# Performance work log

Measured on AMD Instinct MI355X. Metric: run time of the kernel, lower is better.

Reference implementation:

```python
import jax, jax.numpy as jnp
import numpy as np

N, D, E, P, L = 50000, 128, 800000, 9, 3
EPS = 1e-5  # torch nn.LayerNorm default eps


def _layernorm(x, g, b):
    m = jnp.mean(x, axis=-1, keepdims=True)
    v = jnp.mean((x - m) ** 2, axis=-1, keepdims=True)
    return (x - m) * jax.lax.rsqrt(v + EPS) * g + b


def _pol_transform(x, M, onehot):
    # x: (N,d), M: (P,d,d), onehot: (N,P). Equivalent to bmm(x[n] @ M[pol[n]])
    # without materializing the (N,d,d) gathered map tensor.
    return jnp.einsum('nd,np,pdk->nk', x, onehot, M)


def setup_inputs() -> dict:
    key = jax.random.key(0)
    ks = jax.random.split(key, 12)
    s = 1.0 / np.sqrt(D)  # xavier-ish scale
    f32 = jnp.float32
    return {
        'x': jax.random.normal(ks[0], (N, D), f32),
        'edge_index': jax.random.randint(ks[1], (2, E), 0, N),
        'ring_polarities': jax.random.randint(ks[2], (N,), 0, P),
        'Wr': jax.random.normal(ks[3], (L, D, D), f32) * s,          # restriction weights
        'S': jax.random.normal(ks[4], (L, P, D, D), f32) * s,        # send_maps
        'dS': jax.random.normal(ks[5], (L, P, D, D), f32) * 0.01,    # delta_send
        'R': jax.random.normal(ks[6], (L, P, D, D), f32) * s,        # receive_maps
        'dR': jax.random.normal(ks[7], (L, P, D, D), f32) * 0.01,    # delta_receive
        'res_scale': jnp.full((L,), 0.92, f32),
        'W1': jax.random.normal(ks[8], (L, D, D), f32) * s,          # update Linear 1
        'b1': jnp.zeros((L, D), f32),
        'ln_g': jnp.ones((L, D), f32),                               # update LayerNorm
        'ln_b': jnp.zeros((L, D), f32),
        'W2': jax.random.normal(ks[9], (L, D, D), f32) * s,          # update Linear 2
        'b2': jnp.zeros((L, D), f32),
        'norm_g': jnp.ones((L, D), f32),                             # output LayerNorm
        'norm_b': jnp.zeros((L, D), f32),
    }


def reference(x, edge_index, ring_polarities, Wr, S, dS, R, dR, res_scale,
              W1, b1, ln_g, ln_b, W2, b2, norm_g, norm_b):
    src, tgt = edge_index[0], edge_index[1]
    pol = ring_polarities % P
    onehot = jax.nn.one_hot(pol, P, dtype=x.dtype)  # (N,P)
    # deg is accumulated over row(=src) in the original code, then used to
    # normalize the scatter over col(=tgt) -- preserved faithfully.
    deg = jax.ops.segment_sum(jnp.ones((E,), x.dtype), src, num_segments=N)
    deg_norm = (1.0 / jnp.clip(deg, 1.0))[:, None]  # (N,1)

    residual = x
    for l in range(L):
        # send transform: map depends only on src-node polarity, so apply
        # per-node then gather (algebraically identical to per-edge bmm).
        xt = _pol_transform(x, S[l] + dS[l], onehot)          # (N,D)
        msg = xt[src] @ Wr[l].T                               # (E,D) restriction per edge
        agg = jax.ops.segment_sum(msg, tgt, num_segments=N)   # index_add scatter
        # receive transform depends only on tgt polarity; linear, so it
        # commutes with the sum over incoming edges.
        out = _pol_transform(agg, R[l] + dR[l], onehot) * deg_norm
        # update MLP (dropout inactive in eval)
        h = jax.nn.relu(_layernorm(out @ W1[l].T + b1[l], ln_g[l], ln_b[l]))
        out = h @ W2[l].T + b2[l]
        out = res_scale[l] * out + x                           # in==out residual
        x = _layernorm(out, norm_g[l], norm_b[l])
    return x + residual  # stack-level residual (res_proj is None, dims match)
```

## Files before the change

### kernel.cpp

```cpp
#include <hip/hip_runtime.h>
#include <hip/hip_bf16.h>

constexpr int N_ = 50000;
constexpr int D_ = 128;
constexpr int E_ = 800000;
constexpr int P_ = 9;
constexpr int L_ = 3;
constexpr float EPS_ = 1e-5f;

constexpr int TM = 64;
constexpr int CHUNK = 4096;
constexpr int NBK = (E_ + CHUNK - 1) / CHUNK;
constexpr int NBUK = 196;
constexpr int HHALF = 256 * NBK;
constexpr int HTOT = 2 * HHALF;
constexpr int NSB = HTOT / 1024;
constexpr int MAT = L_ * P_;

typedef short bf16x8 __attribute__((ext_vector_type(8)));
typedef float f32x4 __attribute__((ext_vector_type(4)));

#define GLD16(gp, lp)                                                        \
    __builtin_amdgcn_global_load_lds(                                        \
        (const __attribute__((address_space(1))) unsigned int*)(gp),         \
        (__attribute__((address_space(3))) unsigned int*)(lp), 16, 0, 0)

__device__ inline unsigned short f2bf(float f) {
    __hip_bfloat16 h = __float2bfloat16(f);
    return *reinterpret_cast<unsigned short*>(&h);
}
__device__ inline float bflo(unsigned u) { return __uint_as_float(u << 16); }
__device__ inline float bfhi(unsigned u) { return __uint_as_float(u & 0xffff0000u); }
__device__ inline float bf2f(unsigned short h) {
    return __uint_as_float((unsigned)h << 16);
}


__global__ __launch_bounds__(256) void setup_nk(const int* __restrict__ ring,
                                                int* __restrict__ pol,
                                                int* __restrict__ bcnt,
                                                const int* __restrict__ ei,
                                                int* __restrict__ histG) {
    __shared__ int h[P_];
    __shared__ int hT[256], hS[256];
    int blk = blockIdx.x, tid = threadIdx.x;
    if (tid < P_) h[tid] = 0;
    hT[tid] = 0;
    hS[tid] = 0;
    __syncthreads();
    int n = blk * 256 + tid;
    if (n < N_) {
        int p = ring[n] % P_;
        pol[n] = p;
        atomicAdd(&h[p], 1);
    }
    int base = blk * CHUNK;
#pragma unroll
    for (int i = 0; i < CHUNK / 256; ++i) {
        int e = base + tid + i * 256;
        if (e < E_) {
            atomicAdd(&hS[ei[e] >> 8], 1);
            atomicAdd(&hT[ei[E_ + e] >> 8], 1);
        }
    }
    __syncthreads();
    if (tid < P_ && h[tid] > 0) atomicAdd(&bcnt[tid], h[tid]);
    histG[tid * NBK + blk] = hT[tid];
    histG[HHALF + tid * NBK + blk] = hS[tid];
}


__global__ __launch_bounds__(1024) void scanH1(int* __restrict__ a,
                                               int* __restrict__ blkSum) {
    __shared__ int wsum[16];
    int tid = threadIdx.x, lane = tid & 63, wid = tid >> 6;
    int idx = blockIdx.x * 1024 + tid;
    int v = a[idx];
    int inc = v;
#pragma unroll
    for (int o = 1; o < 64; o <<= 1) {
        int t = __shfl_up(inc, o, 64);
        if (lane >= o) inc += t;
    }
    if (lane == 63) wsum[wid] = inc;
    __syncthreads();
    if (tid < 16) {
        int s = wsum[tid];
#pragma unroll
        for (int o = 1; o < 16; o <<= 1) {
            int t = __shfl_up(s, o, 64);
            if (tid >= o) s += t;
        }
        wsum[tid] = s;
    }
    __syncthreads();
    int wexcl = (wid == 0) ? 0 : wsum[wid - 1];
    a[idx] = wexcl + inc - v;
    if (tid == 1023) blkSum[blockIdx.x] = wsum[15];
}

__global__ void scanH2(const int* __restrict__ blkSum, int* __restrict__ blkOff,
                       int* __restrict__ offT, const int* __restrict__ bcnt,
                       int* __restrict__ boff, int* __restrict__ tileOff) {
    if (threadIdx.x != 0) return;
    int run = 0;
    for (int i = 0; i < NSB; ++i) {
        blkOff[i] = run;
        run += blkSum[i];
    }
    offT[N_] = E_;
    boff[0] = 0;
    tileOff[0] = 0;
    for (int p = 0; p < P_; ++p) {
        boff[p + 1] = boff[p] + bcnt[p];
        tileOff[p + 1] = tileOff[p] + (bcnt[p] + TM - 1) / TM;
    }
}

__global__ __launch_bounds__(1024) void scanH3(int* __restrict__ a,
                                               const int* __restrict__ blkOff) {
    int idx = blockIdx.x * 1024 + threadIdx.x;
    a[idx] += blkOff[blockIdx.x];
}


__global__ __launch_bounds__(256) void scatterTS(const int* __restrict__ ei,
                                                 const int* __restrict__ histG,
                                                 unsigned* __restrict__ bufT,
                                                 unsigned char* __restrict__ bufS8) {
    __shared__ int ldsT[256], ldsS[256];
    int blk = blockIdx.x, tid = threadIdx.x;
    ldsT[tid] = histG[tid * NBK + blk];
    ldsS[tid] = histG[HHALF + tid * NBK + blk] - E_;
    __syncthreads();
    int base = blk * CHUNK;
#pragma unroll
    for (int i = 0; i < CHUNK / 256; ++i) {
        int e = base + tid + i * 256;
        if (e < E_) {
            int s = ei[e], t = ei[E_ + e];
            int pT = atomicAdd(&ldsT[t >> 8], 1);
            bufT[pT] = ((unsigned)t << 16) | (unsigned)s;
            int pS = atomicAdd(&ldsS[s >> 8], 1);
            bufS8[pS] = (unsigned char)(s & 255);
        }
    }
}


__global__ __launch_bounds__(256) void finalize3(
    const unsigned* __restrict__ bufT, const unsigned char* __restrict__ bufS8,
    const int* __restrict__ histG, int* __restrict__ offT,
    unsigned short* __restrict__ eSrc, float* __restrict__ dnorm,
    const int* __restrict__ pol, const int* __restrict__ boff,
    int* __restrict__ bcur, int* __restrict__ blist) {
    __shared__ int s0[256];
    __shared__ int s1[256];
    int bb = blockIdx.x, tid = threadIdx.x;

    if (bb < NBUK) {
        int b = bb;
        int start = histG[b * NBK];
        int end = histG[(b + 1) * NBK];
        s0[tid] = 0;
        __syncthreads();
        for (int i = start + tid; i < end; i += 256)
            atomicAdd(&s0[(bufT[i] >> 16) & 255], 1);
        __syncthreads();
        if (tid < 64) {
            int b0 = 4 * tid;
            int v0 = s0[b0], v1 = s0[b0 + 1], v2 = s0[b0 + 2], v3 = s0[b0 + 3];
            int lsum = v0 + v1 + v2 + v3;
            int inc = lsum;
#pragma unroll
            for (int o = 1; o < 64; o <<= 1) {
                int t = __shfl_up(inc, o, 64);
                if (tid >= o) inc += t;
            }
            int excl = inc - lsum;
            s1[b0] = excl;
            s1[b0 + 1] = excl + v0;
            s1[b0 + 2] = excl + v0 + v1;
            s1[b0 + 3] = excl + v0 + v1 + v2;
        }
        __syncthreads();
        int node = (b << 8) + tid;
        if (node < N_) offT[node] = start + s1[tid];
        __syncthreads();
        for (int i = start + tid; i < end; i += 256) {
            unsigned pk = bufT[i];
            int pos = start + atomicAdd(&s1[(pk >> 16) & 255], 1);
            eSrc[pos] = (unsigned short)(pk & 0xFFFF);
        }
    } else if (bb < 2 * NBUK) {
        int b = bb - NBUK;
        int start = histG[HHALF + b * NBK] - E_;
        int end = histG[HHALF + (b + 1) * NBK] - E_;
        s0[tid] = 0;
        __syncthreads();
        for (int i = start + tid; i < end; i += 256) atomicAdd(&s0[bufS8[i]], 1);
        __syncthreads();
        int node = (b << 8) + tid;
        if (node < N_) {
            int dg = s0[tid];
            dnorm[node] = 1.f / (float)(dg > 1 ? dg : 1);
        }
    } else {
        int b = bb - 2 * NBUK;
        if (tid < P_) s0[tid] = 0;
        __syncthreads();
        int n = b * 256 + tid;
        int p = 0, loc = 0;
        bool act = (n < N_);
        if (act) {
            p = pol[n];
            loc = atomicAdd(&s0[p], 1);
        }
        __syncthreads();
        if (tid < P_ && s0[tid] > 0) s1[tid] = atomicAdd(&bcur[tid], s0[tid]);
        __syncthreads();
        if (act) blist[boff[p] + s1[p] + loc] = n;
    }
}


constexpr int GCONV = N_ * D_ / 4 / 256;
constexpr int GS = L_ * P_ * D_ * D_ / 256;
constexpr int GW2 = L_ * D_ * D_ / 256;
constexpr int GSPL = (MAT + 6) * 16384 / 256;
constexpr int GPREP = GCONV + 1 + GS + GW2 + GSPL;

__global__ __launch_bounds__(256) void prep_all(
    const float* __restrict__ x, unsigned short* __restrict__ xb,
    unsigned short* __restrict__ bufAb, unsigned short* __restrict__ bufBb,
    const float* __restrict__ S, const float* __restrict__ dS,
    unsigned short* __restrict__ Sb,
    const float* __restrict__ W2, unsigned short* __restrict__ W2b,
    const float* __restrict__ R, const float* __restrict__ dR,
    const float* __restrict__ W1, const float* __restrict__ Wr,
    unsigned short* __restrict__ Arh, unsigned short* __restrict__ Arl,
    unsigned short* __restrict__ W1h, unsigned short* __restrict__ W1l,
    unsigned short* __restrict__ Wrth, unsigned short* __restrict__ Wrtl) {
    int b = blockIdx.x, tid = threadIdx.x;
    if (b < GCONV) {
        int i = b * 256 + tid;
        float4 v = ((const float4*)x)[i];
        ushort4 o;
        o.x = f2bf(v.x); o.y = f2bf(v.y); o.z = f2bf(v.z); o.w = f2bf(v.w);
        ((ushort4*)xb)[i] = o;
    } else if (b < GCONV + 1) {
        if (tid < 64) {
            ((unsigned*)(xb + (size_t)N_ * D_))[tid] = 0;
            ((unsigned*)(bufAb + (size_t)N_ * D_))[tid] = 0;
            ((unsigned*)(bufBb + (size_t)N_ * D_))[tid] = 0;
        }
    } else if (b < GCONV + 1 + GS) {
        int idx = (b - GCONV - 1) * 256 + tid;
        int base = idx / (D_ * D_);
        int rem = idx % (D_ * D_);
        int c = rem / D_, d = rem % D_;
        size_t in = (size_t)base * D_ * D_ + (size_t)d * D_ + c;
        Sb[idx] = f2bf(S[in] + dS[in]);
    } else if (b < GCONV + 1 + GS + GW2) {
        int idx = (b - GCONV - 1 - GS) * 256 + tid;
        W2b[idx] = f2bf(W2[idx]);
    } else {
        constexpr int SZ1 = MAT * 16384;
        constexpr int SZ2 = SZ1 + 3 * 16384;
        int idx = (b - GCONV - 1 - GS - GW2) * 256 + tid;
        float v;
        unsigned short* oh;
        unsigned short* ol;
        int j;
        if (idx < SZ1) {
            v = R[idx] + dR[idx];
            oh = Arh; ol = Arl; j = idx;
        } else if (idx < SZ2) {
            j = idx - SZ1;
            v = W1[j];
            oh = W1h; ol = W1l;
        } else {
            j = idx - SZ2;
            int l = j >> 14, rem = j & 16383;
            int d = rem >> 7, i = rem & 127;
            v = Wr[(l << 14) + i * 128 + d];
            oh = Wrth; ol = Wrtl;
        }
        unsigned short h = f2bf(v);
        oh[j] = h;
        ol[j] = f2bf(v - bf2f(h));
    }
}


template <bool APM, bool BPM, bool OUT_SPLIT>
__global__ __launch_bounds__(256) void small_mfma(
    const unsigned short* __restrict__ Ah, const unsigned short* __restrict__ Al,
    const unsigned short* __restrict__ Bh, const unsigned short* __restrict__ Bl,
    unsigned short* __restrict__ Oh, unsigned short* __restrict__ Ol) {
    __shared__ unsigned short stg[(OUT_SPLIT ? 2 : 1) * 64 * 136];
    int tid = threadIdx.x, b = blockIdx.x;
    int mat = b >> 1, rb = b & 1;
    int l = mat / P_;
    size_t aoff = (size_t)(APM ? mat : l) * 16384 + (size_t)rb * 8192;
    size_t boff = (size_t)(BPM ? mat : l) * 16384;
    const unsigned short* ahp = Ah + aoff;
    const unsigned short* alp = Al + aoff;
    const unsigned short* bhp = Bh + boff;
    const unsigned short* blp = Bl + boff;

    int lane = tid & 63, wave = tid >> 6;
    int n = lane & 15, q = lane >> 4;
    int wr = wave * 16;

    f32x4 acc[8];
#pragma unroll
    for (int t = 0; t < 8; ++t) acc[t] = (f32x4){0.f, 0.f, 0.f, 0.f};

    int arow = (wr + n) * 128;
#pragma unroll
    for (int kc = 0; kc < 4; ++kc) {
        int ko = kc * 32 + q * 8;
        bf16x8 avh = *(const bf16x8*)(ahp + arow + ko);
        bf16x8 avl = *(const bf16x8*)(alp + arow + ko);
#pragma unroll
        for (int t = 0; t < 8; ++t) {
            int brow = (t * 16 + n) * 128;
            bf16x8 bvh = *(const bf16x8*)(bhp + brow + ko);
            bf16x8 bvl = *(const bf16x8*)(blp + brow + ko);
            acc[t] = __builtin_amdgcn_mfma_f32_16x16x32_bf16(avh, bvh, acc[t], 0, 0, 0);
            acc[t] = __builtin_amdgcn_mfma_f32_16x16x32_bf16(avh, bvl, acc[t], 0, 0, 0);
            acc[t] = __builtin_amdgcn_mfma_f32_16x16x32_bf16(avl, bvh, acc[t], 0, 0, 0);
        }
    }
#pragma unroll
    for (int t = 0; t < 8; ++t)
#pragma unroll
        for (int r = 0; r < 4; ++r) {
            int row = wr + q * 4 + r;
            float v = acc[t][r];
            unsigned short h = f2bf(v);
            stg[row * 136 + t * 16 + n] = h;
            if constexpr (OUT_SPLIT)
                stg[64 * 136 + row * 136 + t * 16 + n] = f2bf(v - bf2f(h));
        }
    __syncthreads();
    size_t obase = (size_t)mat * 16384 + (size_t)rb * 8192;
#pragma unroll
    for (int i = 0; i < 4; ++i) {
        int c = tid + i * 256;
        int r = c >> 4, off = c & 15;
        *(uint4*)(Oh + obase + r * 128 + off * 8) =
            *(const uint4*)(stg + r * 136 + off * 8);
        if constexpr (OUT_SPLIT)
            *(uint4*)(Ol + obase + r * 128 + off * 8) =
                *(const uint4*)(stg + 64 * 136 + r * 136 + off * 8);
    }
}


__device__ inline void accum_row(float* acc, uint4 r) {
    acc[0] += bflo(r.x); acc[1] += bfhi(r.x);
    acc[2] += bflo(r.y); acc[3] += bfhi(r.y);
    acc[4] += bflo(r.z); acc[5] += bfhi(r.z);
    acc[6] += bflo(r.w); acc[7] += bfhi(r.w);
}

__global__ __launch_bounds__(256) void aggregate_bf(const unsigned short* __restrict__ xt,
                                                    const int* __restrict__ offT,
                                                    const unsigned short* __restrict__ eSrc,
                                                    unsigned short* __restrict__ agg) {
    int nd = blockIdx.x * 4 + (threadIdx.x >> 6);
    if (nd >= N_) return;
    int l = threadIdx.x & 63;
    int g = l >> 4, c16 = l & 15;
    int beg = offT[nd], end = offT[nd + 1];

    float acc[8];
#pragma unroll
    for (int k = 0; k < 8; ++k) acc[k] = 0.f;

    for (int base = beg; base < end; base += 64) {
        int cnt = min(64, end - base);
        int idxv = (l < cnt) ? (int)eSrc[base + l] : 0;
        int steps = (cnt + 3) >> 2;
        int j = 0;
        for (; j + 3 < steps; j += 4) {
            int e0 = 4 * j + g, e1 = e0 + 4, e2 = e0 + 8, e3 = e0 + 12;
            int i0 = __shfl(idxv, e0, 64);
            int i1 = __shfl(idxv, e1, 64);
            int i2 = __shfl(idxv, e2, 64);
            int i3 = __shfl(idxv, e3, 64);
            int r0 = (e0 < cnt) ? i0 : N_;
            int r1 = (e1 < cnt) ? i1 : N_;
            int r2 = (e2 < cnt) ? i2 : N_;
            int r3 = (e3 < cnt) ? i3 : N_;
            uint4 v0 = ((const uint4*)(xt + (size_t)r0 * D_))[c16];
            uint4 v1 = ((const uint4*)(xt + (size_t)r1 * D_))[c16];
            uint4 v2 = ((const uint4*)(xt + (size_t)r2 * D_))[c16];
            uint4 v3 = ((const uint4*)(xt + (size_t)r3 * D_))[c16];
            accum_row(acc, v0);
            accum_row(acc, v1);
            accum_row(acc, v2);
            accum_row(acc, v3);
        }
        for (; j < steps; ++j) {
            int e0 = 4 * j + g;
            int i0 = __shfl(idxv, e0, 64);
            int r0 = (e0 < cnt) ? i0 : N_;
            uint4 v0 = ((const uint4*)(xt + (size_t)r0 * D_))[c16];
            accum_row(acc, v0);
        }
    }
#pragma unroll
    for (int k = 0; k < 8; ++k) {
        acc[k] += __shfl_xor(acc[k], 16, 64);
        acc[k] += __shfl_xor(acc[k], 32, 64);
    }
    if (g == 0) {
        uint4 o;
        o.x = (unsigned)f2bf(acc[0]) | ((unsigned)f2bf(acc[1]) << 16);
        o.y = (unsigned)f2bf(acc[2]) | ((unsigned)f2bf(acc[3]) << 16);
        o.z = (unsigned)f2bf(acc[4]) | ((unsigned)f2bf(acc[5]) << 16);
        o.w = (unsigned)f2bf(acc[6]) | ((unsigned)f2bf(acc[7]) << 16);
        ((uint4*)(agg + (size_t)nd * D_))[c16] = o;
    }
}


__device__ inline void stage_B_async(const unsigned short* __restrict__ B,
                                     unsigned short* sB, int wave, int lane) {
    int rsub = lane >> 4, cl = lane & 15;
#pragma unroll
    for (int j = 0; j < 8; ++j) {
        int seg = wave * 8 + j;
        int row = seg * 4 + rsub;
        GLD16(B + row * 128 + ((cl ^ (row & 15)) << 3), sB + seg * 512);
    }
}

__device__ inline void stage_A_async(const unsigned short* __restrict__ A,
                                     const int* rid, unsigned short* sA,
                                     int wave, int lane) {
    int rsub = lane >> 4, cl = lane & 15;
#pragma unroll
    for (int j = 0; j < 4; ++j) {
        int seg = wave * 4 + j;
        int rloc = seg * 4 + rsub;
        int rw = rid[rloc];
        size_t grow = (rw >= 0) ? (size_t)rw : (size_t)N_;
        GLD16(A + grow * 128 + ((cl ^ (rloc & 15)) << 3), sA + seg * 512);
    }
}


__global__ __launch_bounds__(256) void gemm_xt0(
    const unsigned short* __restrict__ A, const unsigned short* __restrict__ Bw,
    unsigned short* __restrict__ OutB, const int* __restrict__ blist,
    const int* __restrict__ boff, const int* __restrict__ tileOff) {
    __shared__ unsigned short sB[128 * 128];
    __shared__ unsigned short sA[64 * 128];
    __shared__ int rid[TM];
    int tid = threadIdx.x, b = blockIdx.x;
    if (b >= tileOff[P_]) return;
    int pp = 0;
    while (pp < P_ - 1 && b >= tileOff[pp + 1]) ++pp;
    int tb = b - tileOff[pp];
    int cnt = boff[pp + 1] - boff[pp];
    int nrows = min(TM, cnt - tb * TM);
    int rowbase = boff[pp] + tb * TM;

    if (tid < TM)
        rid[tid] = (tid < nrows) ? blist[rowbase + tid] : -1;
    __syncthreads();

    int lane = tid & 63, wave = tid >> 6;
    stage_B_async(Bw + (size_t)pp * D_ * D_, sB, wave, lane);
    stage_A_async(A, rid, sA, wave, lane);
    __syncthreads();

    int n = lane & 15, q = lane >> 4, wr = wave * 16;

    f32x4 acc[8];
#pragma unroll
    for (int t = 0; t < 8; ++t) acc[t] = (f32x4){0.f, 0.f, 0.f, 0.f};
#pragma unroll
    for (int kc = 0; kc < 4; ++kc) {
        int cs = (((kc << 2) + q) ^ n) << 3;
        bf16x8 af = *(const bf16x8*)(sA + (wr + n) * 128 + cs);
#pragma unroll
        for (int t = 0; t < 8; ++t) {
            bf16x8 bf = *(const bf16x8*)(sB + (t * 16 + n) * 128 + cs);
            acc[t] = __builtin_amdgcn_mfma_f32_16x16x32_bf16(af, bf, acc[t], 0, 0, 0);
        }
    }
    __syncthreads();
#pragma unroll
    for (int t = 0; t < 8; ++t)
#pragma unroll
        for (int r = 0; r < 4; ++r) {
            int rl = q * 4 + r;
            int c = ((t * 16 + n) >> 3);
            sA[(wr + rl) * 128 + ((c ^ rl) << 3) + (n & 7)] = f2bf(acc[t][r]);
        }
    __syncthreads();
#pragma unroll
    for (int i = 0; i < 4; ++i) {
        int cth = tid + i * 256;
        int r = cth >> 4, cl = cth & 15;
        int row = rid[r];
        if (row >= 0)
            *(uint4*)(OutB + (size_t)row * D_ + (cl << 3)) =
                *(const uint4*)(sA + r * 128 + ((cl ^ (r & 15)) << 3));
    }
}


template <bool LAST>
__global__ __launch_bounds__(256) void fused_layer(
    const unsigned short* __restrict__ agg, const unsigned short* __restrict__ DmAll,
    const unsigned short* __restrict__ W2b, const unsigned short* __restrict__ SnAll,
    const int* __restrict__ blist, const int* __restrict__ boff,
    const int* __restrict__ tileOff, const float* __restrict__ dnorm,
    const float* __restrict__ b1v, const float* __restrict__ g1v,
    const float* __restrict__ e1v, const float* __restrict__ b2v,
    const float* __restrict__ g2v, const float* __restrict__ e2v,
    const float* __restrict__ rs_ptr, const float* __restrict__ xres,
    const float* __restrict__ x0add, float* __restrict__ OutF,
    unsigned short* __restrict__ OutXt) {
    __shared__ unsigned short sB[128 * 128];
    __shared__ unsigned short sA[64 * 128];
    __shared__ int rid[TM];
    __shared__ float dnRow[TM];

    int tid = threadIdx.x, b = blockIdx.x;
    if (b >= tileOff[P_]) return;
    int pp = 0;
    while (pp < P_ - 1 && b >= tileOff[pp + 1]) ++pp;
    int tb = b - tileOff[pp];
    int cnt = boff[pp + 1] - boff[pp];
    int nrows = min(TM, cnt - tb * TM);
    int rowbase = boff[pp] + tb * TM;

    if (tid < TM) {
        int r = (tid < nrows) ? blist[rowbase + tid] : -1;
        rid[tid] = r;
        dnRow[tid] = (r >= 0) ? dnorm[r] : 1.f;
    }
    __syncthreads();

    int lane = tid & 63, wave = tid >> 6;
    stage_B_async(DmAll + (size_t)pp * D_ * D_, sB, wave, lane);
    stage_A_async(agg, rid, sA, wave, lane);

    int n = lane & 15, q = lane >> 4, wr = wave * 16;

    int rowid[4];
    float dn4[4];
#pragma unroll
    for (int r = 0; r < 4; ++r) {
        int rr = wr + q * 4 + r;
        rowid[r] = rid[rr];
        dn4[r] = dnRow[rr];
    }

    float xr[8][4];
#pragma unroll
    for (int t = 0; t < 8; ++t) {
        int col = t * 16 + n;
#pragma unroll
        for (int r = 0; r < 4; ++r)
            xr[t][r] = (rowid[r] >= 0) ? xres[(size_t)rowid[r] * D_ + col] : 0.f;
    }
    __syncthreads();

    f32x4 acc[8];
#pragma unroll
    for (int t = 0; t < 8; ++t) acc[t] = (f32x4){0.f, 0.f, 0.f, 0.f};
#pragma unroll
    for (int kc = 0; kc < 4; ++kc) {
        int cs = (((kc << 2) + q) ^ n) << 3;
        bf16x8 af = *(const bf16x8*)(sA + (wr + n) * 128 + cs);
#pragma unroll
        for (int t = 0; t < 8; ++t) {
            bf16x8 bf = *(const bf16x8*)(sB + (t * 16 + n) * 128 + cs);
            acc[t] = __builtin_amdgcn_mfma_f32_16x16x32_bf16(af, bf, acc[t], 0, 0, 0);
        }
    }

    {
        float rs1[4] = {0, 0, 0, 0}, rs2[4] = {0, 0, 0, 0};
#pragma unroll
        for (int t = 0; t < 8; ++t) {
            int col = t * 16 + n;
            float bia = b1v[col];
#pragma unroll
            for (int r = 0; r < 4; ++r) {
                float v = dn4[r] * acc[t][r] + bia;
                acc[t][r] = v;
                rs1[r] += v;
                rs2[r] += v * v;
            }
        }
#pragma unroll
        for (int mk = 1; mk < 16; mk <<= 1)
#pragma unroll
            for (int r = 0; r < 4; ++r) {
                rs1[r] += __shfl_xor(rs1[r], mk, 64);
                rs2[r] += __shfl_xor(rs2[r], mk, 64);
            }
        float mr[4], rv[4];
#pragma unroll
        for (int r = 0; r < 4; ++r) {
            float mm = rs1[r] * (1.f / 128.f);
            mr[r] = mm;
            rv[r] = rsqrtf(rs2[r] * (1.f / 128.f) - mm * mm + EPS_);
        }
#pragma unroll
        for (int t = 0; t < 8; ++t) {
            int col = t * 16 + n;
            float gg = g1v[col], bbv = e1v[col];
#pragma unroll
            for (int r = 0; r < 4; ++r)
                acc[t][r] = fmaxf((acc[t][r] - mr[r]) * rv[r] * gg + bbv, 0.f);
        }
    }

    __syncthreads();
    stage_B_async(W2b, sB, wave, lane);
#pragma unroll
    for (int t = 0; t < 8; ++t)
#pragma unroll
        for (int r = 0; r < 4; ++r) {
            int rl = q * 4 + r;
            int c = ((t * 16 + n) >> 3);
            sA[(wr + rl) * 128 + ((c ^ rl) << 3) + (n & 7)] = f2bf(acc[t][r]);
        }
    __syncthreads();

#pragma unroll
    for (int t = 0; t < 8; ++t) acc[t] = (f32x4){0.f, 0.f, 0.f, 0.f};
#pragma unroll
    for (int kc = 0; kc < 4; ++kc) {
        int cs = (((kc << 2) + q) ^ n) << 3;
        bf16x8 af = *(const bf16x8*)(sA + (wr + n) * 128 + cs);
#pragma unroll
        for (int t = 0; t < 8; ++t) {
            bf16x8 bf = *(const bf16x8*)(sB + (t * 16 + n) * 128 + cs);
            acc[t] = __builtin_amdgcn_mfma_f32_16x16x32_bf16(af, bf, acc[t], 0, 0, 0);
        }
    }

    {
        float rs = rs_ptr[0];
        float rs1[4] = {0, 0, 0, 0}, rs2[4] = {0, 0, 0, 0};
#pragma unroll
        for (int t = 0; t < 8; ++t) {
            int col = t * 16 + n;
            float bia = b2v[col];
#pragma unroll
            for (int r = 0; r < 4; ++r) {
                float v = rs * (acc[t][r] + bia) + xr[t][r];
                acc[t][r] = v;
                rs1[r] += v;
                rs2[r] += v * v;
            }
        }
#pragma unroll
        for (int mk = 1; mk < 16; mk <<= 1)
#pragma unroll
            for (int r = 0; r < 4; ++r) {
                rs1[r] += __shfl_xor(rs1[r], mk, 64);
                rs2[r] += __shfl_xor(rs2[r], mk, 64);
            }
        float mr[4], rv[4];
#pragma unroll
        for (int r = 0; r < 4; ++r) {
            float mm = rs1[r] * (1.f / 128.f);
            mr[r] = mm;
            rv[r] = rsqrtf(rs2[r] * (1.f / 128.f) - mm * mm + EPS_);
        }
#pragma unroll
        for (int t = 0; t < 8; ++t) {
            int col = t * 16 + n;
            float gg = g2v[col], bbv = e2v[col];
#pragma unroll
            for (int r = 0; r < 4; ++r) {
                float nv = (acc[t][r] - mr[r]) * rv[r] * gg + bbv;
                if constexpr (LAST) {
                    if (rowid[r] >= 0) nv += x0add[(size_t)rowid[r] * D_ + col];
                }
                acc[t][r] = nv;
                if (rowid[r] >= 0) OutF[(size_t)rowid[r] * D_ + col] = nv;
            }
        }
    }

    if constexpr (!LAST) {
        __syncthreads();
        stage_B_async(SnAll + (size_t)pp * D_ * D_, sB, wave, lane);
#pragma unroll
        for (int t = 0; t < 8; ++t)
#pragma unroll
            for (int r = 0; r < 4; ++r) {
                int rl = q * 4 + r;
                int c = ((t * 16 + n) >> 3);
                sA[(wr + rl) * 128 + ((c ^ rl) << 3) + (n & 7)] = f2bf(acc[t][r]);
            }
        __syncthreads();

#pragma unroll
        for (int t = 0; t < 8; ++t) acc[t] = (f32x4){0.f, 0.f, 0.f, 0.f};
#pragma unroll
        for (int kc = 0; kc < 4; ++kc) {
            int cs = (((kc << 2) + q) ^ n) << 3;
            bf16x8 af = *(const bf16x8*)(sA + (wr + n) * 128 + cs);
#pragma unroll
            for (int t = 0; t < 8; ++t) {
                bf16x8 bf = *(const bf16x8*)(sB + (t * 16 + n) * 128 + cs);
                acc[t] = __builtin_amdgcn_mfma_f32_16x16x32_bf16(af, bf, acc[t], 0, 0, 0);
            }
        }
#pragma unroll
        for (int t = 0; t < 8; ++t)
#pragma unroll
            for (int r = 0; r < 4; ++r) {
                int rl = q * 4 + r;
                int c = ((t * 16 + n) >> 3);
                sA[(wr + rl) * 128 + ((c ^ rl) << 3) + (n & 7)] = f2bf(acc[t][r]);
            }
        __syncthreads();
#pragma unroll
        for (int i = 0; i < 4; ++i) {
            int cth = tid + i * 256;
            int r = cth >> 4, cl = cth & 15;
            int row = rid[r];
            if (row >= 0)
                *(uint4*)(OutXt + (size_t)row * D_ + (cl << 3)) =
                    *(const uint4*)(sA + r * 128 + ((cl ^ (r & 15)) << 3));
        }
    }
}


extern "C" void kernel_launch(void* const* d_in, const int* in_sizes, int n_in,
                              void* d_out, int out_size, void* d_ws, size_t ws_size,
                              hipStream_t stream) {
    const float* x0 = (const float*)d_in[0];
    const int* ei = (const int*)d_in[1];
    const int* ring = (const int*)d_in[2];
    const float* Wr = (const float*)d_in[3];
    const float* S = (const float*)d_in[4];
    const float* dS = (const float*)d_in[5];
    const float* R = (const float*)d_in[6];
    const float* dR = (const float*)d_in[7];
    const float* rsc = (const float*)d_in[8];
    const float* W1 = (const float*)d_in[9];
    const float* b1 = (const float*)d_in[10];
    const float* lng = (const float*)d_in[11];
    const float* lnb = (const float*)d_in[12];
    const float* W2 = (const float*)d_in[13];
    const float* b2 = (const float*)d_in[14];
    const float* ng = (const float*)d_in[15];
    const float* nb = (const float*)d_in[16];
    float* out = (float*)d_out;

    char* w = (char*)d_ws;
    auto alloc = [&](size_t bytes) {
        char* p = w;
        w += (bytes + 15) & ~(size_t)15;
        return p;
    };
    unsigned short* xb = (unsigned short*)alloc((size_t)(N_ + 1) * D_ * 2);
    unsigned short* bufAb = (unsigned short*)alloc((size_t)(N_ + 1) * D_ * 2);
    unsigned short* bufBb = (unsigned short*)alloc((size_t)(N_ + 1) * D_ * 2);
    float* xbuf = (float*)alloc((size_t)N_ * D_ * 4);
    unsigned short* Sb = (unsigned short*)alloc((size_t)L_ * P_ * D_ * D_ * 2);
    unsigned short* Dmb = (unsigned short*)alloc((size_t)L_ * P_ * D_ * D_ * 2);
    unsigned short* W2b = (unsigned short*)alloc((size_t)L_ * D_ * D_ * 2);
    unsigned short* Arh = (unsigned short*)alloc((size_t)MAT * 16384 * 2);
    unsigned short* Arl = (unsigned short*)alloc((size_t)MAT * 16384 * 2);
    unsigned short* W1h = (unsigned short*)alloc((size_t)3 * 16384 * 2);
    unsigned short* W1l = (unsigned short*)alloc((size_t)3 * 16384 * 2);
    unsigned short* Wrth = (unsigned short*)alloc((size_t)3 * 16384 * 2);
    unsigned short* Wrtl = (unsigned short*)alloc((size_t)3 * 16384 * 2);
    unsigned short* T1th = (unsigned short*)alloc((size_t)MAT * 16384 * 2);
    unsigned short* T1tl = (unsigned short*)alloc((size_t)MAT * 16384 * 2);
    float* dnorm = (float*)alloc((size_t)N_ * 4);
    int* histG = (int*)alloc((size_t)HTOT * 4);
    unsigned* bufT = (unsigned*)alloc((size_t)E_ * 4);
    unsigned char* bufS8 = (unsigned char*)alloc((size_t)E_);
    unsigned short* eSrc = (unsigned short*)alloc((size_t)E_ * 2);
    int* offT = (int*)alloc((size_t)(N_ + 1) * 4);
    int* pol = (int*)alloc((size_t)N_ * 4);
    int* boff = (int*)alloc((size_t)(P_ + 1) * 4);
    int* tileOff = (int*)alloc((size_t)(P_ + 1) * 4);
    int* blist = (int*)alloc((size_t)N_ * 4);
    int* blkSum = (int*)alloc((size_t)NSB * 4);
    int* blkOff = (int*)alloc((size_t)NSB * 4);
    int* bcnt = (int*)alloc((size_t)2 * P_ * 4);
    int* bcur = bcnt + P_;

    hipMemsetAsync(bcnt, 0, (size_t)2 * P_ * 4, stream);

    const int BTILES = N_ / TM + P_;

    setup_nk<<<NBK, 256, 0, stream>>>(ring, pol, bcnt, ei, histG);
    scanH1<<<NSB, 1024, 0, stream>>>(histG, blkSum);
    scanH2<<<1, 64, 0, stream>>>(blkSum, blkOff, offT, bcnt, boff, tileOff);
    scanH3<<<NSB, 1024, 0, stream>>>(histG, blkOff);
    scatterTS<<<NBK, 256, 0, stream>>>(ei, histG, bufT, bufS8);
    finalize3<<<3 * NBUK, 256, 0, stream>>>(bufT, bufS8, histG, offT, eSrc, dnorm,
                                            pol, boff, bcur, blist);
    prep_all<<<GPREP, 256, 0, stream>>>(x0, xb, bufAb, bufBb, S, dS, Sb, W2, W2b,
                                        R, dR, W1, Wr, Arh, Arl, W1h, W1l, Wrth, Wrtl);
    small_mfma<false, true, true><<<2 * MAT, 256, 0, stream>>>(
        W1h, W1l, Arh, Arl, T1th, T1tl);
    small_mfma<true, false, false><<<2 * MAT, 256, 0, stream>>>(
        T1th, T1tl, Wrth, Wrtl, Dmb, nullptr);

    gemm_xt0<<<BTILES, 256, 0, stream>>>(xb, Sb, bufAb, blist, boff, tileOff);

    for (int l = 0; l < L_; ++l) {
        const size_t lPDD = (size_t)l * P_ * D_ * D_;
        const size_t lDD = (size_t)l * D_ * D_;
        const size_t lD = (size_t)l * D_;
        aggregate_bf<<<N_ / 4, 256, 0, stream>>>(bufAb, offT, eSrc, bufBb);
        const float* xr = (l == 0) ? x0 : xbuf;
        if (l < L_ - 1) {
            fused_layer<false><<<BTILES, 256, 0, stream>>>(
                bufBb, Dmb + lPDD, W2b + lDD, Sb + lPDD + (size_t)P_ * D_ * D_,
                blist, boff, tileOff, dnorm,
                b1 + lD, lng + lD, lnb + lD, b2 + lD, ng + lD, nb + lD,
                rsc + l, xr, nullptr, xbuf, bufAb);
        } else {
            fused_layer<true><<<BTILES, 256, 0, stream>>>(
                bufBb, Dmb + lPDD, W2b + lDD, nullptr,
                blist, boff, tileOff, dnorm,
                b1 + lD, lng + lD, lnb + lD, b2 + lD, ng + lD, nb + lD,
                rsc + l, xr, x0, out, nullptr);
        }
    }
}
```

Baseline: 378.6 us.

## Store node features in polarity-sorted order and read GEMM weights from global

Nodes are renumbered into polarity-bucket order through a new perm array. The features, residual buffer, degree norms and edge source indices are all permuted once during prep, and aggregation writes its result at the permuted position. As a result the GEMM tiles load contiguous rows instead of gathering through blist. The per-tile weight matrices are now read straight from global memory rather than staged in LDS, and most block-wide barriers are replaced by per-wave waits, since each wave only touches its own rows. This removes the indirect gathers and cuts LDS use. The cost is repeated uncached-in-LDS weight reads per wave and an extra permutation pass over the edges.

New measurement: 464.0 us. 22.5% more time.

```diff
diff --git a/kernel.cpp b/kernel.cpp
--- a/kernel.cpp
+++ b/kernel.cpp
@@ -153,7 +153,7 @@
     const int* __restrict__ histG, int* __restrict__ offT,
     unsigned short* __restrict__ eSrc, float* __restrict__ dnorm,
     const int* __restrict__ pol, const int* __restrict__ boff,
-    int* __restrict__ bcur, int* __restrict__ blist) {
+    int* __restrict__ bcur, int* __restrict__ blist, int* __restrict__ perm) {
     __shared__ int s0[256];
     __shared__ int s1[256];
     int bb = blockIdx.x, tid = threadIdx.x;
@@ -219,20 +219,29 @@
         __syncthreads();
         if (tid < P_ && s0[tid] > 0) s1[tid] = atomicAdd(&bcur[tid], s0[tid]);
         __syncthreads();
-        if (act) blist[boff[p] + s1[p] + loc] = n;
+        if (act) {
+            int pos = boff[p] + s1[p] + loc;
+            blist[pos] = n;
+            perm[n] = pos;
+        }
     }
 }
 
 
 constexpr int GCONV = N_ * D_ / 4 / 256;
+constexpr int GDN = (N_ + 255) / 256;
+constexpr int GER = (E_ + 255) / 256;
 constexpr int GS = L_ * P_ * D_ * D_ / 256;
 constexpr int GW2 = L_ * D_ * D_ / 256;
 constexpr int GSPL = (MAT + 6) * 16384 / 256;
-constexpr int GPREP = GCONV + 1 + GS + GW2 + GSPL;
+constexpr int GPREP = GCONV + 1 + GDN + GER + GS + GW2 + GSPL;
 
 __global__ __launch_bounds__(256) void prep_all(
-    const float* __restrict__ x, unsigned short* __restrict__ xb,
-    unsigned short* __restrict__ bufAb, unsigned short* __restrict__ bufBb,
+    const float* __restrict__ x, const int* __restrict__ perm,
+    const int* __restrict__ blist, unsigned short* __restrict__ xbP,
+    float* __restrict__ xbufP, unsigned short* __restrict__ bufAb,
+    const float* __restrict__ dnorm, float* __restrict__ dnormp,
+    unsigned short* __restrict__ eSrc,
     const float* __restrict__ S, const float* __restrict__ dS,
     unsigned short* __restrict__ Sb,
     const float* __restrict__ W2, unsigned short* __restrict__ W2b,
@@ -244,30 +253,35 @@
     int b = blockIdx.x, tid = threadIdx.x;
     if (b < GCONV) {
         int i = b * 256 + tid;
+        int n = i >> 5, g4 = i & 31;
+        int pr = perm[n];
         float4 v = ((const float4*)x)[i];
         ushort4 o;
         o.x = f2bf(v.x); o.y = f2bf(v.y); o.z = f2bf(v.z); o.w = f2bf(v.w);
-        ((ushort4*)xb)[i] = o;
+        ((ushort4*)(xbP + (size_t)pr * D_))[g4] = o;
+        ((float4*)(xbufP + (size_t)pr * D_))[g4] = v;
     } else if (b < GCONV + 1) {
-        if (tid < 64) {
-            ((unsigned*)(xb + (size_t)N_ * D_))[tid] = 0;
-            ((unsigned*)(bufAb + (size_t)N_ * D_))[tid] = 0;
-            ((unsigned*)(bufBb + (size_t)N_ * D_))[tid] = 0;
-        }
-    } else if (b < GCONV + 1 + GS) {
-        int idx = (b - GCONV - 1) * 256 + tid;
+        if (tid < 64) ((unsigned*)(bufAb + (size_t)N_ * D_))[tid] = 0;
+    } else if (b < GCONV + 1 + GDN) {
+        int i = (b - GCONV - 1) * 256 + tid;
+        if (i < N_) dnormp[i] = dnorm[blist[i]];
+    } else if (b < GCONV + 1 + GDN + GER) {
+        int e = (b - GCONV - 1 - GDN) * 256 + tid;
+        if (e < E_) eSrc[e] = (unsigned short)perm[eSrc[e]];
+    } else if (b < GCONV + 1 + GDN + GER + GS) {
+        int idx = (b - GCONV - 1 - GDN - GER) * 256 + tid;
         int base = idx / (D_ * D_);
         int rem = idx % (D_ * D_);
         int c = rem / D_, d = rem % D_;
         size_t in = (size_t)base * D_ * D_ + (size_t)d * D_ + c;
         Sb[idx] = f2bf(S[in] + dS[in]);
-    } else if (b < GCONV + 1 + GS + GW2) {
-        int idx = (b - GCONV - 1 - GS) * 256 + tid;
+    } else if (b < GCONV + 1 + GDN + GER + GS + GW2) {
+        int idx = (b - GCONV - 1 - GDN - GER - GS) * 256 + tid;
         W2b[idx] = f2bf(W2[idx]);
     } else {
         constexpr int SZ1 = MAT * 16384;
         constexpr int SZ2 = SZ1 + 3 * 16384;
-        int idx = (b - GCONV - 1 - GS - GW2) * 256 + tid;
+        int idx = (b - GCONV - 1 - GDN - GER - GS - GW2) * 256 + tid;
         float v;
         unsigned short* oh;
         unsigned short* ol;
@@ -369,7 +383,8 @@
 __global__ __launch_bounds__(256) void aggregate_bf(const unsigned short* __restrict__ xt,
                                                     const int* __restrict__ offT,
                                                     const unsigned short* __restrict__ eSrc,
-                                                    unsigned short* __restrict__ agg) {
+                                                    unsigned short* __restrict__ agg,
+                                                    const int* __restrict__ perm) {
     int nd = blockIdx.x * 4 + (threadIdx.x >> 6);
     if (nd >= N_) return;
     int l = threadIdx.x & 63;
@@ -418,49 +433,35 @@
         acc[k] += __shfl_xor(acc[k], 32, 64);
     }
     if (g == 0) {
+        int pnd = perm[nd];
         uint4 o;
         o.x = (unsigned)f2bf(acc[0]) | ((unsigned)f2bf(acc[1]) << 16);
         o.y = (unsigned)f2bf(acc[2]) | ((unsigned)f2bf(acc[3]) << 16);
         o.z = (unsigned)f2bf(acc[4]) | ((unsigned)f2bf(acc[5]) << 16);
         o.w = (unsigned)f2bf(acc[6]) | ((unsigned)f2bf(acc[7]) << 16);
-        ((uint4*)(agg + (size_t)nd * D_))[c16] = o;
-    }
-}
-
-
-__device__ inline void stage_B_async(const unsigned short* __restrict__ B,
-                                     unsigned short* sB, int wave, int lane) {
-    int rsub = lane >> 4, cl = lane & 15;
-#pragma unroll
-    for (int j = 0; j < 8; ++j) {
-        int seg = wave * 8 + j;
-        int row = seg * 4 + rsub;
-        GLD16(B + row * 128 + ((cl ^ (row & 15)) << 3), sB + seg * 512);
-    }
-}
-
-__device__ inline void stage_A_async(const unsigned short* __restrict__ A,
-                                     const int* rid, unsigned short* sA,
-                                     int wave, int lane) {
+        ((uint4*)(agg + (size_t)pnd * D_))[c16] = o;
+    }
+}
+
+
+__device__ inline void stage_A_contig(const unsigned short* __restrict__ A,
+                                      int rowbase, unsigned short* sA,
+                                      int wave, int lane) {
     int rsub = lane >> 4, cl = lane & 15;
 #pragma unroll
     for (int j = 0; j < 4; ++j) {
         int seg = wave * 4 + j;
         int rloc = seg * 4 + rsub;
-        int rw = rid[rloc];
-        size_t grow = (rw >= 0) ? (size_t)rw : (size_t)N_;
-        GLD16(A + grow * 128 + ((cl ^ (rloc & 15)) << 3), sA + seg * 512);
-    }
-}
-
+        GLD16(A + (size_t)(rowbase + rloc) * D_ + ((cl ^ (rloc & 15)) << 3),
+              sA + seg * 512);
+    }
+}
 
 __global__ __launch_bounds__(256) void gemm_xt0(
     const unsigned short* __restrict__ A, const unsigned short* __restrict__ Bw,
-    unsigned short* __restrict__ OutB, const int* __restrict__ blist,
-    const int* __restrict__ boff, const int* __restrict__ tileOff) {
-    __shared__ unsigned short sB[128 * 128];
+    unsigned short* __restrict__ OutB, const int* __restrict__ boff,
+    const int* __restrict__ tileOff) {
     __shared__ unsigned short sA[64 * 128];
-    __shared__ int rid[TM];
     int tid = threadIdx.x, b = blockIdx.x;
     if (b >= tileOff[P_]) return;
     int pp = 0;
@@ -470,16 +471,12 @@
     int nrows = min(TM, cnt - tb * TM);
     int rowbase = boff[pp] + tb * TM;
 
-    if (tid < TM)
-        rid[tid] = (tid < nrows) ? blist[rowbase + tid] : -1;
-    __syncthreads();
-
     int lane = tid & 63, wave = tid >> 6;
-    stage_B_async(Bw + (size_t)pp * D_ * D_, sB, wave, lane);
-    stage_A_async(A, rid, sA, wave, lane);
-    __syncthreads();
+    stage_A_contig(A, rowbase, sA, wave, lane);
+    const unsigned short* Bp = Bw + (size_t)pp * D_ * D_;
 
     int n = lane & 15, q = lane >> 4, wr = wave * 16;
+    __builtin_amdgcn_s_waitcnt(0);
 
     f32x4 acc[8];
 #pragma unroll
@@ -488,51 +485,45 @@
     for (int kc = 0; kc < 4; ++kc) {
         int cs = (((kc << 2) + q) ^ n) << 3;
         bf16x8 af = *(const bf16x8*)(sA + (wr + n) * 128 + cs);
+        int ko = kc * 32 + q * 8;
 #pragma unroll
         for (int t = 0; t < 8; ++t) {
-            bf16x8 bf = *(const bf16x8*)(sB + (t * 16 + n) * 128 + cs);
-            acc[t] = __builtin_amdgcn_mfma_f32_16x16x32_bf16(af, bf, acc[t], 0, 0, 0);
-        }
-    }
-    __syncthreads();
+            bf16x8 bv = *(const bf16x8*)(Bp + (t * 16 + n) * 128 + ko);
+            acc[t] = __builtin_amdgcn_mfma_f32_16x16x32_bf16(af, bv, acc[t], 0, 0, 0);
+        }
+    }
 #pragma unroll
     for (int t = 0; t < 8; ++t)
 #pragma unroll
         for (int r = 0; r < 4; ++r) {
             int rl = q * 4 + r;
-            int c = ((t * 16 + n) >> 3);
+            int c = (t * 16 + n) >> 3;
             sA[(wr + rl) * 128 + ((c ^ rl) << 3) + (n & 7)] = f2bf(acc[t][r]);
         }
-    __syncthreads();
-#pragma unroll
-    for (int i = 0; i < 4; ++i) {
-        int cth = tid + i * 256;
-        int r = cth >> 4, cl = cth & 15;
-        int row = rid[r];
-        if (row >= 0)
-            *(uint4*)(OutB + (size_t)row * D_ + (cl << 3)) =
-                *(const uint4*)(sA + r * 128 + ((cl ^ (r & 15)) << 3));
-    }
-}
-
+    int rl2 = lane >> 2, cb = lane & 3;
+    if (rl2 < nrows - wr) {
+#pragma unroll
+        for (int i = 0; i < 4; ++i) {
+            int c = i * 4 + cb;
+            uint4 v = *(const uint4*)(sA + (wr + rl2) * 128 + ((c ^ rl2) << 3));
+            *(uint4*)(OutB + (size_t)(rowbase + wr + rl2) * D_ + (c << 3)) = v;
+        }
+    }
+}
 
 template <bool LAST>
 __global__ __launch_bounds__(256) void fused_layer(
     const unsigned short* __restrict__ agg, const unsigned short* __restrict__ DmAll,
     const unsigned short* __restrict__ W2b, const unsigned short* __restrict__ SnAll,
-    const int* __restrict__ blist, const int* __restrict__ boff,
-    const int* __restrict__ tileOff, const float* __restrict__ dnorm,
+    const int* __restrict__ boff, const int* __restrict__ tileOff,
+    const int* __restrict__ blist, const float* __restrict__ dnormp,
     const float* __restrict__ b1v, const float* __restrict__ g1v,
     const float* __restrict__ e1v, const float* __restrict__ b2v,
     const float* __restrict__ g2v, const float* __restrict__ e2v,
-    const float* __restrict__ rs_ptr, const float* __restrict__ xres,
-    const float* __restrict__ x0add, float* __restrict__ OutF,
+    const float* __restrict__ rs_ptr, const float* __restrict__ xresP,
+    const float* __restrict__ x0, float* __restrict__ OutF,
     unsigned short* __restrict__ OutXt) {
-    __shared__ unsigned short sB[128 * 128];
     __shared__ unsigned short sA[64 * 128];
-    __shared__ int rid[TM];
-    __shared__ float dnRow[TM];
-
     int tid = threadIdx.x, b = blockIdx.x;
     if (b >= tileOff[P_]) return;
     int pp = 0;
@@ -542,37 +533,16 @@
     int nrows = min(TM, cnt - tb * TM);
     int rowbase = boff[pp] + tb * TM;
 
-    if (tid < TM) {
-        int r = (tid < nrows) ? blist[rowbase + tid] : -1;
-        rid[tid] = r;
-        dnRow[tid] = (r >= 0) ? dnorm[r] : 1.f;
-    }
-    __syncthreads();
-
     int lane = tid & 63, wave = tid >> 6;
-    stage_B_async(DmAll + (size_t)pp * D_ * D_, sB, wave, lane);
-    stage_A_async(agg, rid, sA, wave, lane);
+    stage_A_contig(agg, rowbase, sA, wave, lane);
 
     int n = lane & 15, q = lane >> 4, wr = wave * 16;
-
-    int rowid[4];
+    const unsigned short* Bp = DmAll + (size_t)pp * D_ * D_;
     float dn4[4];
 #pragma unroll
-    for (int r = 0; r < 4; ++r) {
-        int rr = wr + q * 4 + r;
-        rowid[r] = rid[rr];
-        dn4[r] = dnRow[rr];
-    }
-
-    float xr[8][4];
-#pragma unroll
-    for (int t = 0; t < 8; ++t) {
-        int col = t * 16 + n;
-#pragma unroll
-        for (int r = 0; r < 4; ++r)
-            xr[t][r] = (rowid[r] >= 0) ? xres[(size_t)rowid[r] * D_ + col] : 0.f;
-    }
-    __syncthreads();
+    for (int r = 0; r < 4; ++r) dn4[r] = dnormp[rowbase + wr + q * 4 + r];
+
+    __builtin_amdgcn_s_waitcnt(0);
 
     f32x4 acc[8];
 #pragma unroll
@@ -581,10 +551,11 @@
     for (int kc = 0; kc < 4; ++kc) {
         int cs = (((kc << 2) + q) ^ n) << 3;
         bf16x8 af = *(const bf16x8*)(sA + (wr + n) * 128 + cs);
+        int ko = kc * 32 + q * 8;
 #pragma unroll
         for (int t = 0; t < 8; ++t) {
-            bf16x8 bf = *(const bf16x8*)(sB + (t * 16 + n) * 128 + cs);
-            acc[t] = __builtin_amdgcn_mfma_f32_16x16x32_bf16(af, bf, acc[t], 0, 0, 0);
+            bf16x8 bv = *(const bf16x8*)(Bp + (t * 16 + n) * 128 + ko);
+            acc[t] = __builtin_amdgcn_mfma_f32_16x16x32_bf16(af, bv, acc[t], 0, 0, 0);
         }
     }
 
@@ -626,17 +597,14 @@
         }
     }
 
-    __syncthreads();
-    stage_B_async(W2b, sB, wave, lane);
 #pragma unroll
     for (int t = 0; t < 8; ++t)
 #pragma unroll
         for (int r = 0; r < 4; ++r) {
             int rl = q * 4 + r;
-            int c = ((t * 16 + n) >> 3);
+            int c = (t * 16 + n) >> 3;
             sA[(wr + rl) * 128 + ((c ^ rl) << 3) + (n & 7)] = f2bf(acc[t][r]);
         }
-    __syncthreads();
 
 #pragma unroll
     for (int t = 0; t < 8; ++t) acc[t] = (f32x4){0.f, 0.f, 0.f, 0.f};
@@ -644,10 +612,11 @@
     for (int kc = 0; kc < 4; ++kc) {
         int cs = (((kc << 2) + q) ^ n) << 3;
         bf16x8 af = *(const bf16x8*)(sA + (wr + n) * 128 + cs);
+        int ko = kc * 32 + q * 8;
 #pragma unroll
         for (int t = 0; t < 8; ++t) {
-            bf16x8 bf = *(const bf16x8*)(sB + (t * 16 + n) * 128 + cs);
-            acc[t] = __builtin_amdgcn_mfma_f32_16x16x32_bf16(af, bf, acc[t], 0, 0, 0);
+            bf16x8 bv = *(const bf16x8*)(W2b + (t * 16 + n) * 128 + ko);
+            acc[t] = __builtin_amdgcn_mfma_f32_16x16x32_bf16(af, bv, acc[t], 0, 0, 0);
         }
     }
 
@@ -660,7 +629,9 @@
             float bia = b2v[col];
 #pragma unroll
             for (int r = 0; r < 4; ++r) {
-                float v = rs * (acc[t][r] + bia) + xr[t][r];
+                int row = wr + q * 4 + r;
+                float v = rs * (acc[t][r] + bia) +
+                          xresP[(size_t)(rowbase + row) * D_ + col];
                 acc[t][r] = v;
                 rs1[r] += v;
                 rs2[r] += v * v;
@@ -680,45 +651,64 @@
             mr[r] = mm;
             rv[r] = rsqrtf(rs2[r] * (1.f / 128.f) - mm * mm + EPS_);
         }
-#pragma unroll
-        for (int t = 0; t < 8; ++t) {
-            int col = t * 16 + n;
-            float gg = g2v[col], bbv = e2v[col];
+        if constexpr (LAST) {
+            int rowid[4];
 #pragma unroll
             for (int r = 0; r < 4; ++r) {
-                float nv = (acc[t][r] - mr[r]) * rv[r] * gg + bbv;
-                if constexpr (LAST) {
-                    if (rowid[r] >= 0) nv += x0add[(size_t)rowid[r] * D_ + col];
+                int rl = wr + q * 4 + r;
+                rowid[r] = (rl < nrows) ? blist[rowbase + rl] : -1;
+            }
+#pragma unroll
+            for (int t = 0; t < 8; ++t) {
+                int col = t * 16 + n;
+                float gg = g2v[col], bbv = e2v[col];
+#pragma unroll
+                for (int r = 0; r < 4; ++r) {
+                    if (rowid[r] >= 0) {
+                        float nv = (acc[t][r] - mr[r]) * rv[r] * gg + bbv +
+                                   x0[(size_t)rowid[r] * D_ + col];
+                        OutF[(size_t)rowid[r] * D_ + col] = nv;
+                    }
                 }
-                acc[t][r] = nv;
-                if (rowid[r] >= 0) OutF[(size_t)rowid[r] * D_ + col] = nv;
+            }
+        } else {
+#pragma unroll
+            for (int t = 0; t < 8; ++t) {
+                int col = t * 16 + n;
+                float gg = g2v[col], bbv = e2v[col];
+#pragma unroll
+                for (int r = 0; r < 4; ++r) {
+                    int row = wr + q * 4 + r;
+                    float nv = (acc[t][r] - mr[r]) * rv[r] * gg + bbv;
+                    acc[t][r] = nv;
+                    if (row < nrows)
+                        OutF[(size_t)(rowbase + row) * D_ + col] = nv;
+                }
             }
         }
     }
 
     if constexpr (!LAST) {
-        __syncthreads();
-        stage_B_async(SnAll + (size_t)pp * D_ * D_, sB, wave, lane);
+        const unsigned short* Sn = SnAll + (size_t)pp * D_ * D_;
 #pragma unroll
         for (int t = 0; t < 8; ++t)
 #pragma unroll
             for (int r = 0; r < 4; ++r) {
                 int rl = q * 4 + r;
-                int c = ((t * 16 + n) >> 3);
+                int c = (t * 16 + n) >> 3;
                 sA[(wr + rl) * 128 + ((c ^ rl) << 3) + (n & 7)] = f2bf(acc[t][r]);
             }
-        __syncthreads();
-
 #pragma unroll
         for (int t = 0; t < 8; ++t) acc[t] = (f32x4){0.f, 0.f, 0.f, 0.f};
 #pragma unroll
         for (int kc = 0; kc < 4; ++kc) {
             int cs = (((kc << 2) + q) ^ n) << 3;
             bf16x8 af = *(const bf16x8*)(sA + (wr + n) * 128 + cs);
+            int ko = kc * 32 + q * 8;
 #pragma unroll
             for (int t = 0; t < 8; ++t) {
-                bf16x8 bf = *(const bf16x8*)(sB + (t * 16 + n) * 128 + cs);
-                acc[t] = __builtin_amdgcn_mfma_f32_16x16x32_bf16(af, bf, acc[t], 0, 0, 0);
+                bf16x8 bv = *(const bf16x8*)(Sn + (t * 16 + n) * 128 + ko);
+                acc[t] = __builtin_amdgcn_mfma_f32_16x16x32_bf16(af, bv, acc[t], 0, 0, 0);
             }
         }
 #pragma unroll
@@ -726,18 +716,17 @@
 #pragma unroll
             for (int r = 0; r < 4; ++r) {
                 int rl = q * 4 + r;
-                int c = ((t * 16 + n) >> 3);
+                int c = (t * 16 + n) >> 3;
                 sA[(wr + rl) * 128 + ((c ^ rl) << 3) + (n & 7)] = f2bf(acc[t][r]);
             }
-        __syncthreads();
-#pragma unroll
-        for (int i = 0; i < 4; ++i) {
-            int cth = tid + i * 256;
-            int r = cth >> 4, cl = cth & 15;
-            int row = rid[r];
-            if (row >= 0)
-                *(uint4*)(OutXt + (size_t)row * D_ + (cl << 3)) =
-                    *(const uint4*)(sA + r * 128 + ((cl ^ (r & 15)) << 3));
+        int rl2 = lane >> 2, cb = lane & 3;
+        if (rl2 < nrows - wr) {
+#pragma unroll
+            for (int i = 0; i < 4; ++i) {
+                int c = i * 4 + cb;
+                uint4 v = *(const uint4*)(sA + (wr + rl2) * 128 + ((c ^ rl2) << 3));
+                *(uint4*)(OutXt + (size_t)(rowbase + wr + rl2) * D_ + (c << 3)) = v;
+            }
         }
     }
 }
@@ -771,10 +760,11 @@
         w += (bytes + 15) & ~(size_t)15;
         return p;
     };
-    unsigned short* xb = (unsigned short*)alloc((size_t)(N_ + 1) * D_ * 2);
-    unsigned short* bufAb = (unsigned short*)alloc((size_t)(N_ + 1) * D_ * 2);
-    unsigned short* bufBb = (unsigned short*)alloc((size_t)(N_ + 1) * D_ * 2);
-    float* xbuf = (float*)alloc((size_t)N_ * D_ * 4);
+    const size_t NP = (size_t)(N_ + 64);
+    unsigned short* xbP = (unsigned short*)alloc(NP * D_ * 2);
+    unsigned short* bufAb = (unsigned short*)alloc(NP * D_ * 2);
+    unsigned short* bufBb = (unsigned short*)alloc(NP * D_ * 2);
+    float* xbufP = (float*)alloc(NP * D_ * 4);
     unsigned short* Sb = (unsigned short*)alloc((size_t)L_ * P_ * D_ * D_ * 2);
     unsigned short* Dmb = (unsigned short*)alloc((size_t)L_ * P_ * D_ * D_ * 2);
     unsigned short* W2b = (unsigned short*)alloc((size_t)L_ * D_ * D_ * 2);
@@ -787,6 +777,7 @@
     unsigned short* T1th = (unsigned short*)alloc((size_t)MAT * 16384 * 2);
     unsigned short* T1tl = (unsigned short*)alloc((size_t)MAT * 16384 * 2);
     float* dnorm = (float*)alloc((size_t)N_ * 4);
+    float* dnormp = (float*)alloc(NP * 4);
     int* histG = (int*)alloc((size_t)HTOT * 4);
     unsigned* bufT = (unsigned*)alloc((size_t)E_ * 4);
     unsigned char* bufS8 = (unsigned char*)alloc((size_t)E_);
@@ -796,6 +787,7 @@
     int* boff = (int*)alloc((size_t)(P_ + 1) * 4);
     int* tileOff = (int*)alloc((size_t)(P_ + 1) * 4);
     int* blist = (int*)alloc((size_t)N_ * 4);
+    int* perm = (int*)alloc((size_t)N_ * 4);
     int* blkSum = (int*)alloc((size_t)NSB * 4);
     int* blkOff = (int*)alloc((size_t)NSB * 4);
     int* bcnt = (int*)alloc((size_t)2 * P_ * 4);
@@ -811,34 +803,34 @@
     scanH3<<<NSB, 1024, 0, stream>>>(histG, blkOff);
     scatterTS<<<NBK, 256, 0, stream>>>(ei, histG, bufT, bufS8);
     finalize3<<<3 * NBUK, 256, 0, stream>>>(bufT, bufS8, histG, offT, eSrc, dnorm,
-                                            pol, boff, bcur, blist);
-    prep_all<<<GPREP, 256, 0, stream>>>(x0, xb, bufAb, bufBb, S, dS, Sb, W2, W2b,
+                                            pol, boff, bcur, blist, perm);
+    prep_all<<<GPREP, 256, 0, stream>>>(x0, perm, blist, xbP, xbufP, bufAb,
+                                        dnorm, dnormp, eSrc, S, dS, Sb, W2, W2b,
                                         R, dR, W1, Wr, Arh, Arl, W1h, W1l, Wrth, Wrtl);
     small_mfma<false, true, true><<<2 * MAT, 256, 0, stream>>>(
         W1h, W1l, Arh, Arl, T1th, T1tl);
     small_mfma<true, false, false><<<2 * MAT, 256, 0, stream>>>(
         T1th, T1tl, Wrth, Wrtl, Dmb, nullptr);
 
-    gemm_xt0<<<BTILES, 256, 0, stream>>>(xb, Sb, bufAb, blist, boff, tileOff);
+    gemm_xt0<<<BTILES, 256, 0, stream>>>(xbP, Sb, bufAb, boff, tileOff);
 
     for (int l = 0; l < L_; ++l) {
         const size_t lPDD = (size_t)l * P_ * D_ * D_;
         const size_t lDD = (size_t)l * D_ * D_;
         const size_t lD = (size_t)l * D_;
-        aggregate_bf<<<N_ / 4, 256, 0, stream>>>(bufAb, offT, eSrc, bufBb);
-        const float* xr = (l == 0) ? x0 : xbuf;
+        aggregate_bf<<<N_ / 4, 256, 0, stream>>>(bufAb, offT, eSrc, bufBb, perm);
         if (l < L_ - 1) {
             fused_layer<false><<<BTILES, 256, 0, stream>>>(
                 bufBb, Dmb + lPDD, W2b + lDD, Sb + lPDD + (size_t)P_ * D_ * D_,
-                blist, boff, tileOff, dnorm,
+                boff, tileOff, blist, dnormp,
                 b1 + lD, lng + lD, lnb + lD, b2 + lD, ng + lD, nb + lD,
-                rsc + l, xr, nullptr, xbuf, bufAb);
+                rsc + l, xbufP, nullptr, xbufP, bufAb);
         } else {
             fused_layer<true><<<BTILES, 256, 0, stream>>>(
                 bufBb, Dmb + lPDD, W2b + lDD, nullptr,
-                blist, boff, tileOff, dnorm,
+                boff, tileOff, blist, dnormp,
                 b1 + lD, lng + lD, lnb + lD, b2 + lD, ng + lD, nb + lD,
-                rsc + l, xr, x0, out, nullptr);
-        }
-    }
-}
+                rsc + l, xbufP, x0, out, nullptr);
+        }
+    }
+}
```
